# Kernel optimization log

Measured on AMD Instinct MI355X. Metric: run time of the kernel, lower is better.

Reference implementation:

```python
import jax, jax.numpy as jnp
import numpy as np

D_M, D_K, D_V, HEADS = 1024, 64, 64, 16
B, S = 2, 2048


def setup_inputs() -> dict:
    key = jax.random.key(0)
    ks = jax.random.split(key, 5)
    x = jax.random.normal(ks[0], (B, S, D_M), dtype=jnp.float32)
    # per-head projection weights (original deep-copies one rand init per head;
    # we give each head independent weights, matching the per-head param structure)
    Wk = jax.random.uniform(ks[1], (HEADS, D_M, D_K), dtype=jnp.float32)
    Wq = jax.random.uniform(ks[2], (HEADS, D_M, D_K), dtype=jnp.float32)
    Wv = jax.random.uniform(ks[3], (HEADS, D_M, D_V), dtype=jnp.float32)
    Wo = jax.random.uniform(ks[4], (HEADS * D_V, D_M), dtype=jnp.float32)
    return {"x": x, "Wk": Wk, "Wq": Wq, "Wv": Wv, "Wo": Wo}


def reference(x, Wk, Wq, Wv, Wo):
    # per-head QKV projections, batched over heads: [B,H,S,d]
    q = jnp.einsum("bsm,hmk->bhsk", x, Wq)
    k = jnp.einsum("bsm,hmk->bhsk", x, Wk)
    v = jnp.einsum("bsm,hmv->bhsv", x, Wv)
    scale = 1.0 / jnp.sqrt(jnp.asarray(q.shape[-1], dtype=q.dtype))
    scores = jnp.einsum("bhsk,bhtk->bhst", q, k) * scale  # [B,H,S,S]
    attn = jax.nn.softmax(scores, axis=-1)
    ctx = jnp.einsum("bhst,bhtv->bhsv", attn, v)  # [B,H,S,d_v]
    # concat heads -> [B,S,H*d_v], then output projection
    ctx = jnp.transpose(ctx, (0, 2, 1, 3)).reshape(x.shape[0], x.shape[1], -1)
    return jnp.einsum("bsc,cm->bsm", ctx, Wo)
```

## Files before the change

### kernel.cpp

```cpp
#include <hip/hip_runtime.h>
#include <hip/hip_bf16.h>
#include <stdint.h>

#define DM   1024
#define DKV  64
#define HEADS 16
#define BATCH 2
#define SEQ  2048
#define BS   (BATCH*SEQ)
#define BHD  (BATCH*HEADS)

typedef __attribute__((ext_vector_type(8))) short bf16x8;
typedef __attribute__((ext_vector_type(4))) short bf16x4;
typedef __attribute__((ext_vector_type(4))) float f32x4;

__device__ inline unsigned fb(float f) { union { float f; unsigned u; } v; v.f = f; return v.u; }

__device__ inline unsigned short bf16_rtn(float f) {
  unsigned u = fb(f);
  unsigned r = u + 0x7fffu + ((u >> 16) & 1u);
  return (unsigned short)(r >> 16);
}
__device__ inline float bf16_to_f(unsigned short h) {
  union { unsigned u; float f; } v; v.u = ((unsigned)h) << 16; return v.f;
}
__device__ inline void split_bf16(float x, unsigned short& hi, unsigned short& lo) {
  hi = bf16_rtn(x);
  lo = bf16_rtn(x - bf16_to_f(hi));
}
__device__ inline unsigned pack2_bf16(float lo_elem, float hi_elem) {
  return __builtin_amdgcn_perm(fb(hi_elem) + 0x8000u, fb(lo_elem) + 0x8000u, 0x07060302u);
}

__device__ inline float fast_exp2(float x) {
#if __has_builtin(__builtin_amdgcn_exp2f)
  return __builtin_amdgcn_exp2f(x);
#else
  return exp2f(x);
#endif
}

__device__ inline f32x4 mfma16x16x16_bf16(bf16x4 a, bf16x4 b, f32x4 c) {
#if __has_builtin(__builtin_amdgcn_mfma_f32_16x16x16bf16_1k)
  return __builtin_amdgcn_mfma_f32_16x16x16bf16_1k(a, b, c, 0, 0, 0);
#else
  asm volatile("v_mfma_f32_16x16x16_bf16 %0, %1, %2, %0" : "+v"(c) : "v"(a), "v"(b));
  return c;
#endif
}

__device__ inline void stage16(const unsigned short* g, unsigned short* lds_base, int lane) {
#if __has_builtin(__builtin_amdgcn_global_load_lds)
  __builtin_amdgcn_global_load_lds((__attribute__((address_space(1))) void*)(g),
                                   (__attribute__((address_space(3))) void*)(lds_base),
                                   16, 0, 0);
#else
  *(bf16x8*)(lds_base + lane * 8) = *(const bf16x8*)g;
#endif
}

__device__ inline int swz(int row, int chunk) {
  return row * 64 + (((chunk ^ (row & 7)) & 7) << 3);
}

__global__ void prep(const float* __restrict__ x,
                     const float* __restrict__ Wq, const float* __restrict__ Wk,
                     const float* __restrict__ Wv, const float* __restrict__ Wo,
                     unsigned short* __restrict__ xh, unsigned short* __restrict__ xl,
                     unsigned short* __restrict__ Wh, unsigned short* __restrict__ Wl,
                     unsigned short* __restrict__ WoT) {
  __shared__ float tile[64][65];
  const int bid = blockIdx.x;
  const int t = threadIdx.x;

  if (bid < 2048) {
    int i = (bid * 256 + t) * 8;
    bf16x8 oh, ol;
    #pragma unroll
    for (int j = 0; j < 8; ++j) {
      unsigned short hi, lo;
      split_bf16(x[i + j], hi, lo);
      oh[j] = (short)hi; ol[j] = (short)lo;
    }
    *(bf16x8*)(xh + i) = oh;
    *(bf16x8*)(xl + i) = ol;
    return;
  }
  if (bid < 2816) {
    int b2 = bid - 2048;
    int p = b2 >> 8, h = (b2 >> 4) & 15, mt = b2 & 15;
    const float* W = (p == 0) ? Wq : (p == 1) ? Wk : Wv;
    const float* src = W + (size_t)h * (DM * DKV);
    int m0 = mt * 64;
    #pragma unroll
    for (int pass = 0; pass < 16; ++pass) {
      int row = pass * 4 + (t >> 6), col = t & 63;
      tile[row][col] = src[(size_t)(m0 + row) * DKV + col];
    }
    __syncthreads();
    int cbase = p * 1024 + h * 64;
    #pragma unroll
    for (int pass = 0; pass < 16; ++pass) {
      int krow = pass * 4 + (t >> 6), mcol = t & 63;
      unsigned short hi, lo;
      split_bf16(tile[mcol][krow], hi, lo);
      size_t idx = (size_t)(cbase + krow) * DM + m0 + mcol;
      Wh[idx] = hi; Wl[idx] = lo;
    }
    return;
  }
  {
    int b3 = bid - 2816;
    int ib = b3 >> 4, jb = b3 & 15;
    #pragma unroll
    for (int pass = 0; pass < 16; ++pass) {
      int row = pass * 4 + (t >> 6), col = t & 63;
      tile[row][col] = Wo[(size_t)(ib * 64 + row) * DM + jb * 64 + col];
    }
    __syncthreads();
    #pragma unroll
    for (int pass = 0; pass < 16; ++pass) {
      int a = pass * 4 + (t >> 6), b = t & 63;
      WoT[(size_t)(jb * 64 + a) * DM + ib * 64 + b] = bf16_rtn(tile[b][a]);
    }
  }
}

__global__ __launch_bounds__(256, 4)
void gemm_qkv(const unsigned short* __restrict__ Ah, const unsigned short* __restrict__ Al,
              const unsigned short* __restrict__ Bh, const unsigned short* __restrict__ Bl,
              unsigned short* __restrict__ Qh, unsigned short* __restrict__ Ql,
              unsigned short* __restrict__ Kh, unsigned short* __restrict__ Kl,
              unsigned short* __restrict__ Vt) {
  __shared__ unsigned short smem[16384];
  const int tid = threadIdx.x;
  const int w = tid >> 6, lane = tid & 63;
  const int quad = lane >> 4, l16 = lane & 15;
  const int wm = w >> 1, wn = w & 1;
  const int bid = blockIdx.x;
  const int r4s = lane >> 2, c4s = lane & 3;
  const int csY = c4s ^ (r4s & 3);

  if (bid < 512) {
    unsigned short* AsH = smem;
    unsigned short* AsL = smem + 4096;
    unsigned short* BsH = smem + 8192;
    unsigned short* BsL = smem + 12288;
    const int bn = bid & 15, bm = bid >> 4;

    f32x4 acc[4][4];
    #pragma unroll
    for (int i = 0; i < 4; ++i)
      #pragma unroll
      for (int j = 0; j < 4; ++j) acc[i][j] = (f32x4){0.f, 0.f, 0.f, 0.f};

    const size_t offA = (size_t)(bm * 128 + w * 32 + r4s) * DM + csY * 8;
    const size_t offB = (size_t)(bn * 128 + w * 32 + r4s) * DM + csY * 8;

    for (int kk = 0; kk < DM / 32; ++kk) {
      stage16(Ah + offA + kk * 32,           AsH + (w * 32) * 32,      lane);
      stage16(Ah + offA + kk * 32 + 16 * DM, AsH + (w * 32 + 16) * 32, lane);
      stage16(Al + offA + kk * 32,           AsL + (w * 32) * 32,      lane);
      stage16(Al + offA + kk * 32 + 16 * DM, AsL + (w * 32 + 16) * 32, lane);
      stage16(Bh + offB + kk * 32,           BsH + (w * 32) * 32,      lane);
      stage16(Bh + offB + kk * 32 + 16 * DM, BsH + (w * 32 + 16) * 32, lane);
      stage16(Bl + offB + kk * 32,           BsL + (w * 32) * 32,      lane);
      stage16(Bl + offB + kk * 32 + 16 * DM, BsL + (w * 32 + 16) * 32, lane);
      asm volatile("s_waitcnt vmcnt(0)" ::: "memory");
      __syncthreads();
      bf16x8 afh[4], afl[4], bfh[4], bfl[4];
      #pragma unroll
      for (int mt = 0; mt < 4; ++mt) {
        int row = wm * 64 + mt * 16 + l16;
        int ad = row * 32 + (((quad ^ (row & 3)) & 3) << 3);
        afh[mt] = *(const bf16x8*)(AsH + ad);
        afl[mt] = *(const bf16x8*)(AsL + ad);
      }
      #pragma unroll
      for (int nt = 0; nt < 4; ++nt) {
        int row = wn * 64 + nt * 16 + l16;
        int ad = row * 32 + (((quad ^ (row & 3)) & 3) << 3);
        bfh[nt] = *(const bf16x8*)(BsH + ad);
        bfl[nt] = *(const bf16x8*)(BsL + ad);
      }
      #pragma unroll
      for (int mt = 0; mt < 4; ++mt)
        #pragma unroll
        for (int nt = 0; nt < 4; ++nt) {
          acc[mt][nt] = __builtin_amdgcn_mfma_f32_16x16x32_bf16(afh[mt], bfh[nt], acc[mt][nt], 0, 0, 0);
          acc[mt][nt] = __builtin_amdgcn_mfma_f32_16x16x32_bf16(afh[mt], bfl[nt], acc[mt][nt], 0, 0, 0);
          acc[mt][nt] = __builtin_amdgcn_mfma_f32_16x16x32_bf16(afl[mt], bfh[nt], acc[mt][nt], 0, 0, 0);
        }
      __syncthreads();
    }

    const float SCL = 0.18033688011112042f;
    #pragma unroll
    for (int mt = 0; mt < 4; ++mt) {
      int m_g = bm * 128 + wm * 64 + mt * 16 + quad * 4;
      #pragma unroll
      for (int nt = 0; nt < 4; ++nt) {
        int n_g = bn * 128 + wn * 64 + nt * 16 + l16;
        int p = n_g >> 10, h = (n_g >> 6) & 15, k = n_g & 63;
        #pragma unroll
        for (int r = 0; r < 4; ++r) {
          int row = m_g + r;
          int b = row >> 11, s = row & 2047;
          int bh = b * HEADS + h;
          float v = acc[mt][nt][r];
          size_t idx = ((size_t)(bh * SEQ + s)) * DKV + k;
          unsigned short hi, lo;
          if (p == 0) {
            split_bf16(v * SCL, hi, lo);
            Qh[idx] = hi; Ql[idx] = lo;
          } else {
            split_bf16(v, hi, lo);
            Kh[idx] = hi; Kl[idx] = lo;
          }
        }
      }
    }
  } else {
    unsigned short* As = smem;
    unsigned short* Bs = smem + 2048;
    const int vid = bid - 512;
    const int bn = vid & 7, bm = vid >> 3;
    const unsigned short* Bt = Bh + (size_t)2048 * DM;

    f32x4 acc[2][4];
    #pragma unroll
    for (int i = 0; i < 2; ++i)
      #pragma unroll
      for (int j = 0; j < 4; ++j) acc[i][j] = (f32x4){0.f, 0.f, 0.f, 0.f};

    const size_t offA = (size_t)(bm * 64 + w * 16 + r4s) * DM + csY * 8;
    const size_t offB = (size_t)(bn * 128 + w * 32 + r4s) * DM + csY * 8;

    for (int kk = 0; kk < DM / 32; ++kk) {
      stage16(Ah + offA + kk * 32,           As + (w * 16) * 32,      lane);
      stage16(Bt + offB + kk * 32,           Bs + (w * 32) * 32,      lane);
      stage16(Bt + offB + kk * 32 + 16 * DM, Bs + (w * 32 + 16) * 32, lane);
      asm volatile("s_waitcnt vmcnt(0)" ::: "memory");
      __syncthreads();
      bf16x8 af[2], bfr[4];
      #pragma unroll
      for (int mt = 0; mt < 2; ++mt) {
        int row = wm * 32 + mt * 16 + l16;
        af[mt] = *(const bf16x8*)(As + row * 32 + (((quad ^ (row & 3)) & 3) << 3));
      }
      #pragma unroll
      for (int nt = 0; nt < 4; ++nt) {
        int row = wn * 64 + nt * 16 + l16;
        bfr[nt] = *(const bf16x8*)(Bs + row * 32 + (((quad ^ (row & 3)) & 3) << 3));
      }
      #pragma unroll
      for (int mt = 0; mt < 2; ++mt)
        #pragma unroll
        for (int nt = 0; nt < 4; ++nt)
          acc[mt][nt] = __builtin_amdgcn_mfma_f32_16x16x32_bf16(af[mt], bfr[nt], acc[mt][nt], 0, 0, 0);
      __syncthreads();
    }

    #pragma unroll
    for (int mt = 0; mt < 2; ++mt) {
      int m_g = bm * 64 + wm * 32 + mt * 16 + quad * 4;
      #pragma unroll
      for (int nt = 0; nt < 4; ++nt) {
        int n_g = bn * 128 + wn * 64 + nt * 16 + l16;
        int h = n_g >> 6, k = n_g & 63;
        #pragma unroll
        for (int r = 0; r < 4; ++r) {
          int row = m_g + r;
          int b = row >> 11, s = row & 2047;
          int bh = b * HEADS + h;
          Vt[((size_t)(bh * DKV + k)) * SEQ + s] = bf16_rtn(acc[mt][nt][r]);
        }
      }
    }
  }
}

__global__ __launch_bounds__(256, 2)
void flash(const unsigned short* __restrict__ Qh, const unsigned short* __restrict__ Ql,
           const unsigned short* __restrict__ Kh, const unsigned short* __restrict__ Kl,
           const unsigned short* __restrict__ Vt, unsigned short* __restrict__ ctx) {
  __shared__ unsigned short KtH[3][64 * 64], KtL[3][64 * 64], Vts[2][64 * 64];
  const int tid = threadIdx.x;
  const int w = tid >> 6, lane = tid & 63, quad = lane >> 4, l16 = lane & 15;
  const int bh = blockIdx.x;
  const int q0 = blockIdx.y * 128;
  const int NT = SEQ / 64;

  bf16x8 qfh[2][2], qfl[2][2];
  #pragma unroll
  for (int qt = 0; qt < 2; ++qt) {
    int qrow = q0 + w * 32 + qt * 16 + l16;
    size_t base = ((size_t)(bh * SEQ + qrow)) * DKV + quad * 8;
    qfh[qt][0] = *(const bf16x8*)(Qh + base);
    qfh[qt][1] = *(const bf16x8*)(Qh + base + 32);
    qfl[qt][0] = *(const bf16x8*)(Ql + base);
    qfl[qt][1] = *(const bf16x8*)(Ql + base + 32);
  }

  float m_run[2] = {-1e30f, -1e30f};
  float l_run[2] = {0.f, 0.f};
  f32x4 acc[2][4];
  #pragma unroll
  for (int qt = 0; qt < 2; ++qt)
    #pragma unroll
    for (int vt = 0; vt < 4; ++vt) acc[qt][vt] = (f32x4){0.f, 0.f, 0.f, 0.f};

  const int srow = w * 16 + (lane >> 3);
  const int csrc = (lane & 7) ^ (lane >> 3);
  const unsigned short* kh_src = Kh + ((size_t)(bh * SEQ) + srow) * DKV + csrc * 8;
  const unsigned short* kl_src = Kl + ((size_t)(bh * SEQ) + srow) * DKV + csrc * 8;
  const unsigned short* v_src  = Vt + ((size_t)(bh * DKV) + srow) * SEQ + csrc * 8;

  #define STAGE_K(buf, kt0)                                                     \
    do {                                                                        \
      unsigned short* dH = &KtH[buf][(w * 16) * 64];                            \
      unsigned short* dL = &KtL[buf][(w * 16) * 64];                            \
      stage16(kh_src + (size_t)(kt0) * 64 * DKV,           dH,       lane);     \
      stage16(kh_src + (size_t)(kt0) * 64 * DKV + 8 * DKV, dH + 512, lane);     \
      stage16(kl_src + (size_t)(kt0) * 64 * DKV,           dL,       lane);     \
      stage16(kl_src + (size_t)(kt0) * 64 * DKV + 8 * DKV, dL + 512, lane);     \
    } while (0)
  #define STAGE_V(buf, kt0)                                                     \
    do {                                                                        \
      unsigned short* dV = &Vts[buf][(w * 16) * 64];                            \
      stage16(v_src + (kt0) * 64,           dV,       lane);                    \
      stage16(v_src + (kt0) * 64 + 8 * SEQ, dV + 512, lane);                    \
    } while (0)

  #define QK_HALF(STV, KHP, KLP, MT0)                                           \
    _Pragma("unroll")                                                           \
    for (int mt = (MT0); mt < (MT0) + 2; ++mt) {                                \
      int rowA = mt * 16 + l16;                                                 \
      bf16x8 kah0 = *(const bf16x8*)((KHP) + swz(rowA, quad));                  \
      bf16x8 kah1 = *(const bf16x8*)((KHP) + swz(rowA, quad + 4));              \
      bf16x8 kal0 = *(const bf16x8*)((KLP) + swz(rowA, quad));                  \
      bf16x8 kal1 = *(const bf16x8*)((KLP) + swz(rowA, quad + 4));              \
      _Pragma("unroll")                                                         \
      for (int qt = 0; qt < 2; ++qt) {                                          \
        f32x4 c = (f32x4){0.f, 0.f, 0.f, 0.f};                                  \
        c = __builtin_amdgcn_mfma_f32_16x16x32_bf16(kah0, qfh[qt][0], c, 0, 0, 0); \
        c = __builtin_amdgcn_mfma_f32_16x16x32_bf16(kah1, qfh[qt][1], c, 0, 0, 0); \
        c = __builtin_amdgcn_mfma_f32_16x16x32_bf16(kah0, qfl[qt][0], c, 0, 0, 0); \
        c = __builtin_amdgcn_mfma_f32_16x16x32_bf16(kah1, qfl[qt][1], c, 0, 0, 0); \
        c = __builtin_amdgcn_mfma_f32_16x16x32_bf16(kal0, qfh[qt][0], c, 0, 0, 0); \
        c = __builtin_amdgcn_mfma_f32_16x16x32_bf16(kal1, qfh[qt][1], c, 0, 0, 0); \
        (STV)[mt][qt] = c;                                                      \
      }                                                                         \
    }

  #define SM_QT(QT)                                                             \
    {                                                                           \
      float cm = -1e30f;                                                        \
      _Pragma("unroll")                                                         \
      for (int mt = 0; mt < 4; ++mt)                                            \
        _Pragma("unroll")                                                       \
        for (int r = 0; r < 4; ++r) cm = fmaxf(cm, st[mt][QT][r]);              \
      if (!__all(cm <= m_run[QT] + 8.0f)) {                                     \
        cm = fmaxf(cm, __shfl_xor(cm, 16));                                     \
        cm = fmaxf(cm, __shfl_xor(cm, 32));                                     \
        float mn = fmaxf(cm, m_run[QT]);                                        \
        float alpha = fast_exp2(m_run[QT] - mn);                                \
        m_run[QT] = mn;                                                         \
        l_run[QT] *= alpha;                                                     \
        _Pragma("unroll")                                                       \
        for (int vt = 0; vt < 4; ++vt) acc[QT][vt] = acc[QT][vt] * alpha;       \
      }                                                                         \
      float mn = m_run[QT];                                                     \
      float ssum = 0.f;                                                         \
      _Pragma("unroll")                                                         \
      for (int mt = 0; mt < 4; ++mt) {                                          \
        float p0 = fast_exp2(st[mt][QT][0] - mn);                               \
        float p1 = fast_exp2(st[mt][QT][1] - mn);                               \
        float p2 = fast_exp2(st[mt][QT][2] - mn);                               \
        float p3 = fast_exp2(st[mt][QT][3] - mn);                               \
        ssum += (p0 + p1) + (p2 + p3);                                          \
        union { bf16x4 v; unsigned u2[2]; } pk;                                 \
        pk.u2[0] = pack2_bf16(p0, p1);                                          \
        pk.u2[1] = pack2_bf16(p2, p3);                                          \
        pb[QT][mt] = pk.v;                                                      \
      }                                                                         \
      l_run[QT] += ssum;                                                        \
    }

  #define PV_ALL(VSP)                                                           \
    _Pragma("unroll")                                                           \
    for (int vt = 0; vt < 4; ++vt)                                              \
      _Pragma("unroll")                                                         \
      for (int mt = 0; mt < 4; ++mt) {                                          \
        int row = vt * 16 + l16;                                                \
        int addr = row * 64 + ((((mt * 2 + (quad >> 1)) ^ (row & 7)) & 7) << 3) + (quad & 1) * 4; \
        bf16x4 va = *(const bf16x4*)((VSP) + addr);                             \
        _Pragma("unroll")                                                       \
        for (int qt = 0; qt < 2; ++qt)                                          \
          acc[qt][vt] = mfma16x16x16_bf16(va, pb[qt][mt], acc[qt][vt]);         \
      }

  STAGE_K(0, 0);
  STAGE_V(0, 0);
  STAGE_K(1, 1);
  STAGE_K(2, 2);
  asm volatile("s_waitcnt vmcnt(4)" ::: "memory");
  __builtin_amdgcn_s_barrier();
  __builtin_amdgcn_sched_barrier(0);

  f32x4 st[4][2];
  __builtin_amdgcn_s_setprio(1);
  QK_HALF(st, KtH[0], KtL[0], 0);
  QK_HALF(st, KtH[0], KtL[0], 2);
  __builtin_amdgcn_s_setprio(0);
  __builtin_amdgcn_s_barrier();
  __builtin_amdgcn_sched_barrier(0);

  #pragma unroll 2
  for (int t = 0; t < NT - 1; ++t) {
    STAGE_V((t + 1) & 1, t + 1);
    if (t + 3 < NT) STAGE_K(t % 3, t + 3);

    const int kslot = (t + 1) % 3;
    const unsigned short* kHn = KtH[kslot];
    const unsigned short* kLn = KtL[kslot];
    const unsigned short* vS  = Vts[t & 1];

    bf16x4 pb[2][4];
    f32x4 stn[4][2];
    SM_QT(0);
    __builtin_amdgcn_s_setprio(1);
    QK_HALF(stn, kHn, kLn, 0);
    __builtin_amdgcn_s_setprio(0);
    SM_QT(1);
    __builtin_amdgcn_s_setprio(1);
    QK_HALF(stn, kHn, kLn, 2);
    PV_ALL(vS);
    __builtin_amdgcn_s_setprio(0);

    #pragma unroll
    for (int mt = 0; mt < 4; ++mt)
      #pragma unroll
      for (int qt = 0; qt < 2; ++qt) st[mt][qt] = stn[mt][qt];

    if (t < NT - 3) {
      asm volatile("s_waitcnt vmcnt(4)" ::: "memory");
    } else {
      asm volatile("s_waitcnt vmcnt(0)" ::: "memory");
    }
    __builtin_amdgcn_s_barrier();
    __builtin_amdgcn_sched_barrier(0);
  }

  {
    bf16x4 pb[2][4];
    SM_QT(0);
    SM_QT(1);
    PV_ALL(Vts[(NT - 1) & 1]);
  }
  #undef STAGE_K
  #undef STAGE_V
  #undef QK_HALF
  #undef SM_QT
  #undef PV_ALL

  int h = bh & 15, b = bh >> 4;
  #pragma unroll
  for (int qt = 0; qt < 2; ++qt) {
    float lt = l_run[qt];
    lt += __shfl_xor(lt, 16);
    lt += __shfl_xor(lt, 32);
    float inv = 1.0f / lt;
    int bs = b * SEQ + q0 + w * 32 + qt * 16 + l16;
    #pragma unroll
    for (int vt = 0; vt < 4; ++vt) {
      union { bf16x4 v; unsigned u2[2]; } pk;
      pk.u2[0] = pack2_bf16(acc[qt][vt][0] * inv, acc[qt][vt][1] * inv);
      pk.u2[1] = pack2_bf16(acc[qt][vt][2] * inv, acc[qt][vt][3] * inv);
      *(bf16x4*)(ctx + (size_t)bs * DM + h * 64 + vt * 16 + quad * 4) = pk.v;
    }
  }
}

__global__ __launch_bounds__(256, 2)
void gemm_out(const unsigned short* __restrict__ A, const unsigned short* __restrict__ Bt,
              float* __restrict__ out) {
  __shared__ unsigned short As[64 * 64];
  __shared__ unsigned short Bs[128 * 64];
  const int tid = threadIdx.x;
  const int w = tid >> 6, lane = tid & 63;
  const int quad = lane >> 4, l16 = lane & 15;
  const int wm = w >> 1, wn = w & 1;
  const int bn = blockIdx.x, bm = blockIdx.y;

  f32x4 acc[2][4];
  #pragma unroll
  for (int i = 0; i < 2; ++i)
    #pragma unroll
    for (int j = 0; j < 4; ++j) acc[i][j] = (f32x4){0.f, 0.f, 0.f, 0.f};

  const int r8 = lane >> 3, c8 = lane & 7;
  const int cs = c8 ^ r8;
  const size_t offA = (size_t)(bm * 64 + w * 16 + r8) * DM + cs * 8;
  const size_t offB = (size_t)(bn * 128 + w * 32 + r8) * DM + cs * 8;

  for (int kk = 0; kk < DM / 64; ++kk) {
    #pragma unroll
    for (int ps = 0; ps < 2; ++ps)
      stage16(A + offA + kk * 64 + ps * 8 * DM, As + (w * 16 + ps * 8) * 64, lane);
    #pragma unroll
    for (int ps = 0; ps < 4; ++ps)
      stage16(Bt + offB + kk * 64 + ps * 8 * DM, Bs + (w * 32 + ps * 8) * 64, lane);
    asm volatile("s_waitcnt vmcnt(0)" ::: "memory");
    __syncthreads();
    #pragma unroll
    for (int ks = 0; ks < 2; ++ks) {
      bf16x8 af[2], bfr[4];
      #pragma unroll
      for (int mt = 0; mt < 2; ++mt) {
        int row = wm * 32 + mt * 16 + l16;
        af[mt] = *(const bf16x8*)(As + row * 64 + ((((ks * 4 + quad) ^ (row & 7)) & 7) << 3));
      }
      #pragma unroll
      for (int nt = 0; nt < 4; ++nt) {
        int row = wn * 64 + nt * 16 + l16;
        bfr[nt] = *(const bf16x8*)(Bs + row * 64 + ((((ks * 4 + quad) ^ (row & 7)) & 7) << 3));
      }
      #pragma unroll
      for (int mt = 0; mt < 2; ++mt)
        #pragma unroll
        for (int nt = 0; nt < 4; ++nt)
          acc[mt][nt] = __builtin_amdgcn_mfma_f32_16x16x32_bf16(af[mt], bfr[nt], acc[mt][nt], 0, 0, 0);
    }
    __syncthreads();
  }

  #pragma unroll
  for (int mt = 0; mt < 2; ++mt) {
    int m_g = bm * 64 + wm * 32 + mt * 16 + quad * 4;
    #pragma unroll
    for (int nt = 0; nt < 4; ++nt) {
      int n_g = bn * 128 + wn * 64 + nt * 16 + l16;
      #pragma unroll
      for (int r = 0; r < 4; ++r)
        out[(size_t)(m_g + r) * DM + n_g] = acc[mt][nt][r];
    }
  }
}

extern "C" void kernel_launch(void* const* d_in, const int* in_sizes, int n_in,
                              void* d_out, int out_size, void* d_ws, size_t ws_size,
                              hipStream_t stream) {
  const float* x  = (const float*)d_in[0];
  const float* Wk = (const float*)d_in[1];
  const float* Wq = (const float*)d_in[2];
  const float* Wv = (const float*)d_in[3];
  const float* Wo = (const float*)d_in[4];
  float* out = (float*)d_out;

  unsigned short* xh  = (unsigned short*)d_ws;
  unsigned short* xl  = xh  + (size_t)BS * DM;
  unsigned short* Wh  = xl  + (size_t)BS * DM;
  unsigned short* Wl  = Wh  + (size_t)3 * DM * DM;
  unsigned short* WoT = Wl  + (size_t)3 * DM * DM;
  unsigned short* Qh  = WoT + (size_t)DM * DM;
  unsigned short* Ql  = Qh  + (size_t)BHD * SEQ * DKV;
  unsigned short* Kh  = Ql  + (size_t)BHD * SEQ * DKV;
  unsigned short* Kl  = Kh  + (size_t)BHD * SEQ * DKV;
  unsigned short* Vtb = Kl  + (size_t)BHD * SEQ * DKV;
  unsigned short* ctx = Vtb + (size_t)BHD * SEQ * DKV;

  prep<<<3072, 256, 0, stream>>>(x, Wq, Wk, Wv, Wo, xh, xl, Wh, Wl, WoT);
  gemm_qkv<<<1024, 256, 0, stream>>>(xh, xl, Wh, Wl, Qh, Ql, Kh, Kl, Vtb);
  flash<<<dim3(BHD, SEQ / 128), 256, 0, stream>>>(Qh, Ql, Kh, Kl, Vtb, ctx);
  gemm_out<<<dim3(8, 64), 256, 0, stream>>>(ctx, WoT, out);
}
```

Before: 237.3 us.

## Double-buffer LDS staging in QKV projection GEMM to overlap loads with MFMA

Adds a second LDS buffer to both the Q/K and V branches of the QKV projection GEMM. The next k-slice is prefetched while MFMAs run on the current one, replacing the load-wait-compute serialization. This doubles LDS to 64 KB per block and lowers the launch_bounds occupancy hint from 4 to 2 blocks per CU, so less latency hiding comes from other waves.

```diff
diff --git a/kernel.cpp b/kernel.cpp
--- a/kernel.cpp
+++ b/kernel.cpp
@@ -126,13 +126,13 @@
   }
 }
 
-__global__ __launch_bounds__(256, 4)
+__global__ __launch_bounds__(256, 2)
 void gemm_qkv(const unsigned short* __restrict__ Ah, const unsigned short* __restrict__ Al,
               const unsigned short* __restrict__ Bh, const unsigned short* __restrict__ Bl,
               unsigned short* __restrict__ Qh, unsigned short* __restrict__ Ql,
               unsigned short* __restrict__ Kh, unsigned short* __restrict__ Kl,
               unsigned short* __restrict__ Vt) {
-  __shared__ unsigned short smem[16384];
+  __shared__ unsigned short smem[32768];
   const int tid = threadIdx.x;
   const int w = tid >> 6, lane = tid & 63;
   const int quad = lane >> 4, l16 = lane & 15;
@@ -142,10 +142,6 @@
   const int csY = c4s ^ (r4s & 3);
 
   if (bid < 512) {
-    unsigned short* AsH = smem;
-    unsigned short* AsL = smem + 4096;
-    unsigned short* BsH = smem + 8192;
-    unsigned short* BsL = smem + 12288;
     const int bn = bid & 15, bm = bid >> 4;
 
     f32x4 acc[4][4];
@@ -157,17 +153,32 @@
     const size_t offA = (size_t)(bm * 128 + w * 32 + r4s) * DM + csY * 8;
     const size_t offB = (size_t)(bn * 128 + w * 32 + r4s) * DM + csY * 8;
 
+    #define QK_STAGE(slot, kk0)                                                    \
+      do {                                                                         \
+        unsigned short* S = smem + (slot) * 16384;                                 \
+        stage16(Ah + offA + (kk0) * 32,           S + (w * 32) * 32,        lane); \
+        stage16(Ah + offA + (kk0) * 32 + 16 * DM, S + (w * 32 + 16) * 32,   lane); \
+        stage16(Al + offA + (kk0) * 32,           S + 4096 + (w * 32) * 32, lane); \
+        stage16(Al + offA + (kk0) * 32 + 16 * DM, S + 4096 + (w * 32 + 16) * 32, lane); \
+        stage16(Bh + offB + (kk0) * 32,           S + 8192 + (w * 32) * 32, lane); \
+        stage16(Bh + offB + (kk0) * 32 + 16 * DM, S + 8192 + (w * 32 + 16) * 32, lane); \
+        stage16(Bl + offB + (kk0) * 32,           S + 12288 + (w * 32) * 32, lane); \
+        stage16(Bl + offB + (kk0) * 32 + 16 * DM, S + 12288 + (w * 32 + 16) * 32, lane); \
+      } while (0)
+
+    QK_STAGE(0, 0);
+    asm volatile("s_waitcnt vmcnt(0)" ::: "memory");
+    __syncthreads();
+
     for (int kk = 0; kk < DM / 32; ++kk) {
-      stage16(Ah + offA + kk * 32,           AsH + (w * 32) * 32,      lane);
-      stage16(Ah + offA + kk * 32 + 16 * DM, AsH + (w * 32 + 16) * 32, lane);
-      stage16(Al + offA + kk * 32,           AsL + (w * 32) * 32,      lane);
-      stage16(Al + offA + kk * 32 + 16 * DM, AsL + (w * 32 + 16) * 32, lane);
-      stage16(Bh + offB + kk * 32,           BsH + (w * 32) * 32,      lane);
-      stage16(Bh + offB + kk * 32 + 16 * DM, BsH + (w * 32 + 16) * 32, lane);
-      stage16(Bl + offB + kk * 32,           BsL + (w * 32) * 32,      lane);
-      stage16(Bl + offB + kk * 32 + 16 * DM, BsL + (w * 32 + 16) * 32, lane);
-      asm volatile("s_waitcnt vmcnt(0)" ::: "memory");
-      __syncthreads();
+      const int cb = kk & 1;
+      if (kk + 1 < DM / 32) QK_STAGE(cb ^ 1, kk + 1);
+
+      const unsigned short* AsH = smem + cb * 16384;
+      const unsigned short* AsL = AsH + 4096;
+      const unsigned short* BsH = AsH + 8192;
+      const unsigned short* BsL = AsH + 12288;
+
       bf16x8 afh[4], afl[4], bfh[4], bfl[4];
       #pragma unroll
       for (int mt = 0; mt < 4; ++mt) {
@@ -191,8 +202,11 @@
           acc[mt][nt] = __builtin_amdgcn_mfma_f32_16x16x32_bf16(afh[mt], bfl[nt], acc[mt][nt], 0, 0, 0);
           acc[mt][nt] = __builtin_amdgcn_mfma_f32_16x16x32_bf16(afl[mt], bfh[nt], acc[mt][nt], 0, 0, 0);
         }
+
+      asm volatile("s_waitcnt vmcnt(0)" ::: "memory");
       __syncthreads();
     }
+    #undef QK_STAGE
 
     const float SCL = 0.18033688011112042f;
     #pragma unroll
@@ -221,8 +235,6 @@
       }
     }
   } else {
-    unsigned short* As = smem;
-    unsigned short* Bs = smem + 2048;
     const int vid = bid - 512;
     const int bn = vid & 7, bm = vid >> 3;
     const unsigned short* Bt = Bh + (size_t)2048 * DM;
@@ -236,12 +248,25 @@
     const size_t offA = (size_t)(bm * 64 + w * 16 + r4s) * DM + csY * 8;
     const size_t offB = (size_t)(bn * 128 + w * 32 + r4s) * DM + csY * 8;
 
+    #define V_STAGE(slot, kk0)                                                     \
+      do {                                                                         \
+        unsigned short* S = smem + (slot) * 6144;                                  \
+        stage16(Ah + offA + (kk0) * 32,           S + (w * 16) * 32,        lane); \
+        stage16(Bt + offB + (kk0) * 32,           S + 2048 + (w * 32) * 32, lane); \
+        stage16(Bt + offB + (kk0) * 32 + 16 * DM, S + 2048 + (w * 32 + 16) * 32, lane); \
+      } while (0)
+
+    V_STAGE(0, 0);
+    asm volatile("s_waitcnt vmcnt(0)" ::: "memory");
+    __syncthreads();
+
     for (int kk = 0; kk < DM / 32; ++kk) {
-      stage16(Ah + offA + kk * 32,           As + (w * 16) * 32,      lane);
-      stage16(Bt + offB + kk * 32,           Bs + (w * 32) * 32,      lane);
-      stage16(Bt + offB + kk * 32 + 16 * DM, Bs + (w * 32 + 16) * 32, lane);
-      asm volatile("s_waitcnt vmcnt(0)" ::: "memory");
-      __syncthreads();
+      const int cb = kk & 1;
+      if (kk + 1 < DM / 32) V_STAGE(cb ^ 1, kk + 1);
+
+      const unsigned short* As = smem + cb * 6144;
+      const unsigned short* Bs = As + 2048;
+
       bf16x8 af[2], bfr[4];
       #pragma unroll
       for (int mt = 0; mt < 2; ++mt) {
@@ -258,8 +283,11 @@
         #pragma unroll
         for (int nt = 0; nt < 4; ++nt)
           acc[mt][nt] = __builtin_amdgcn_mfma_f32_16x16x32_bf16(af[mt], bfr[nt], acc[mt][nt], 0, 0, 0);
+
+      asm volatile("s_waitcnt vmcnt(0)" ::: "memory");
       __syncthreads();
     }
+    #undef V_STAGE
 
     #pragma unroll
     for (int mt = 0; mt < 2; ++mt) {
```

New measurement: 297.6 us (median of 2 runs). 1.25x slower.
